# Kernel tuning notes

Hardware: AMD Instinct MI355X
Metric: run time of the kernel (lower is better)

Reference implementation:

```python
import jax, jax.numpy as jnp
import numpy as np

B, S, D, H = 2, 2048, 1024, 16
HD = D // H  # head_dim = 64


def setup_inputs() -> dict:
    key = jax.random.key(0)
    ks = jax.random.split(key, 9)
    scale = 0.02
    x = jax.random.normal(ks[0], (B, S, D), dtype=jnp.float32)
    wq = jax.random.normal(ks[1], (D, D), dtype=jnp.float32) * scale
    bq = jnp.zeros((D,), dtype=jnp.float32)
    wk = jax.random.normal(ks[2], (D, D), dtype=jnp.float32) * scale
    bk = jnp.zeros((D,), dtype=jnp.float32)
    wv = jax.random.normal(ks[3], (D, D), dtype=jnp.float32) * scale
    bv = jnp.zeros((D,), dtype=jnp.float32)
    wo = jax.random.normal(ks[4], (D, D), dtype=jnp.float32) * scale
    bo = jnp.zeros((D,), dtype=jnp.float32)
    # causal mask: 1.0 where key position is in the future of query position
    mask = jnp.triu(jnp.ones((S, S), dtype=jnp.float32), k=1)[None, None]  # [1,1,S,S]
    return {"x": x, "wq": wq, "bq": bq, "wk": wk, "bk": bk,
            "wv": wv, "bv": bv, "wo": wo, "bo": bo, "mask": mask}


def reference(x, wq, bq, wk, bk, wv, bv, wo, bo, mask):
    b, s, d = x.shape
    q = (x @ wq + bq).reshape(b, s, H, HD).transpose(0, 2, 1, 3)  # [b,h,s,hd]
    k = (x @ wk + bk).reshape(b, s, H, HD).transpose(0, 2, 1, 3)
    v = (x @ wv + bv).reshape(b, s, H, HD).transpose(0, 2, 1, 3)
    scores = jnp.einsum('bhqd,bhkd->bhqk', q, k) / jnp.sqrt(jnp.float32(HD))
    scores = scores + mask * (-1e9)
    probs = jax.nn.softmax(scores, axis=-1)
    out = jnp.einsum('bhqk,bhkd->bhqd', probs, v)
    out = out.transpose(0, 2, 1, 3).reshape(b, s, d)
    return out @ wo + bo
```

## Files before the change

### kernel.cpp

```cpp
#include <hip/hip_runtime.h>
#include <hip/hip_bf16.h>
#include <cstdint>

#define DEV static __device__ __forceinline__

typedef unsigned short u16t;
typedef __attribute__((ext_vector_type(4))) float f32x4;
typedef __attribute__((ext_vector_type(4))) unsigned short u16x4;
typedef __attribute__((ext_vector_type(8))) unsigned short u16x8;
typedef __attribute__((ext_vector_type(8))) __bf16 bf16x8;

DEV u16t f2bf(float f) {
  unsigned u = __builtin_bit_cast(unsigned, f);
  u += 0x7fffu + ((u >> 16) & 1u);
  return (u16t)(u >> 16);
}
DEV float bf2f(u16t h) {
  unsigned u = ((unsigned)h) << 16;
  return __builtin_bit_cast(float, u);
}

DEV void gload_lds16(const void* g, void* l) {
  __builtin_amdgcn_global_load_lds(
      (const __attribute__((address_space(1))) void*)g,
      (__attribute__((address_space(3))) void*)l, 16, 0, 0);
}

DEV bf16x8 ldsfrag(const u16t* p) {
  return __builtin_bit_cast(bf16x8, *(const u16x8*)p);
}

DEV void bsync() {
  asm volatile("" ::: "memory");
  __builtin_amdgcn_s_barrier();
  asm volatile("" ::: "memory");
}

__global__ __launch_bounds__(256) void k_convert_x(const float* __restrict__ x,
                                                   u16t* __restrict__ xb) {
  int i = (blockIdx.x * 256 + threadIdx.x) * 4;
  f32x4 v = *(const f32x4*)&x[i];
  u16x4 o;
#pragma unroll
  for (int j = 0; j < 4; ++j) o[j] = f2bf(v[j]);
  *(u16x4*)&xb[i] = o;
}

__global__ __launch_bounds__(256) void k_transw(const float* __restrict__ w0,
                                                const float* __restrict__ w1,
                                                const float* __restrict__ w2,
                                                const float* __restrict__ w3,
                                                u16t* __restrict__ qkvT,
                                                u16t* __restrict__ oT) {
  __shared__ float lds[64][68];
  int z = blockIdx.z;
  const float* W = (z == 0) ? w0 : (z == 1) ? w1 : (z == 2) ? w2 : w3;
  u16t* OUT = (z < 3) ? (qkvT + (size_t)z * 1024 * 1024) : oT;
  int k0 = blockIdx.x * 64, n0 = blockIdx.y * 64;
  int t = threadIdx.x;
  int kl = t >> 4, n4 = (t & 15) << 2;
#pragma unroll
  for (int p = 0; p < 4; ++p) {
    f32x4 v = *(const f32x4*)&W[(size_t)(k0 + kl + p * 16) * 1024 + n0 + n4];
    *(f32x4*)&lds[kl + p * 16][n4] = v;
  }
  __syncthreads();
  int nl = t >> 4, k4 = (t & 15) << 2;
#pragma unroll
  for (int p = 0; p < 4; ++p) {
    int n = nl + p * 16;
    u16x4 o;
#pragma unroll
    for (int i = 0; i < 4; ++i) o[i] = f2bf(lds[k4 + i][n]);
    *(u16x4*)&OUT[(size_t)(n0 + n) * 1024 + k0 + k4] = o;
  }
}

template <int MI, bool BF16_OUT, bool VSPLIT>
__global__ __launch_bounds__(256) void k_gemm_bt(const u16t* __restrict__ A,
                                                 const u16t* __restrict__ BT,
                                                 void* __restrict__ Cout,
                                                 const float* __restrict__ b0,
                                                 const float* __restrict__ b1,
                                                 const float* __restrict__ b2,
                                                 u16t* __restrict__ vt,
                                                 int M, int N, int K) {
  __shared__ u16t Al[2][MI * 32 * 64];
  __shared__ u16t Bl[2][128 * 64];
  const int tid = threadIdx.x;
  const int l = tid & 63;
  const int w = tid >> 6;
  const int m0 = blockIdx.x * (MI * 32), n0 = blockIdx.y * 128;
  const int wm = (w >> 1) * (MI * 16), wn = (w & 1) * 64;
  const int lm = l & 15, lh = l >> 4;
  f32x4 acc[MI][4] = {};

  auto stage = [&](int bb, int t) {
    const int k0 = t << 6;
#pragma unroll
    for (int s = 0; s < MI; ++s) {
      int c = s * 256 + tid;
      int row = c >> 3, slot = c & 7;
      int ks = k0 + (((slot ^ (row & 7)) & 7) << 3);
      gload_lds16(A + (size_t)(m0 + row) * K + ks, &Al[bb][c * 8]);
    }
#pragma unroll
    for (int s = 0; s < 4; ++s) {
      int c = s * 256 + tid;
      int row = c >> 3, slot = c & 7;
      int ks = k0 + (((slot ^ (row & 7)) & 7) << 3);
      gload_lds16(BT + (size_t)(n0 + row) * K + ks, &Bl[bb][c * 8]);
    }
  };

  const int nt = K >> 6;
  stage(0, 0);
  for (int t = 0; t < nt; ++t) {
    if (t + 1 < nt) {
      stage((t + 1) & 1, t + 1);
      if (MI == 2)
        asm volatile("s_waitcnt vmcnt(6)" ::: "memory");
      else
        asm volatile("s_waitcnt vmcnt(8)" ::: "memory");
    } else {
      asm volatile("s_waitcnt vmcnt(0)" ::: "memory");
    }
    bsync();
    const int buf = t & 1;

#pragma unroll
    for (int kk = 0; kk < 2; ++kk) {
      bf16x8 af[MI], bfr[4];
#pragma unroll
      for (int i = 0; i < MI; ++i) {
        int ra = wm + i * 16 + lm;
        int sa = (kk * 4 + lh) ^ (ra & 7);
        af[i] = ldsfrag(&Al[buf][ra * 64 + sa * 8]);
      }
#pragma unroll
      for (int i = 0; i < 4; ++i) {
        int rb = wn + i * 16 + lm;
        int sb = (kk * 4 + lh) ^ (rb & 7);
        bfr[i] = ldsfrag(&Bl[buf][rb * 64 + sb * 8]);
      }
#pragma unroll
      for (int i = 0; i < MI; ++i)
#pragma unroll
        for (int j = 0; j < 4; ++j)
          acc[i][j] = __builtin_amdgcn_mfma_f32_16x16x32_bf16(af[i], bfr[j],
                                                              acc[i][j], 0, 0, 0);
    }
    bsync();
  }

  if (!VSPLIT || (n0 + wn) < 2048) {
#pragma unroll
    for (int i = 0; i < MI; ++i) {
      int row = m0 + wm + i * 16 + (lh << 2);
#pragma unroll
      for (int j = 0; j < 4; ++j) {
        int col = n0 + wn + j * 16 + lm;
        const float* bp = (col < 1024) ? b0 : ((col < 2048) ? b1 : b2);
        float bias = bp[col & 1023];
#pragma unroll
        for (int r = 0; r < 4; ++r) {
          float v = acc[i][j][r] + bias;
          if (BF16_OUT)
            ((u16t*)Cout)[(size_t)(row + r) * N + col] = f2bf(v);
          else
            ((float*)Cout)[(size_t)(row + r) * N + col] = v;
        }
      }
    }
  } else {
#pragma unroll
    for (int i = 0; i < MI; ++i) {
      int row = m0 + wm + i * 16 + (lh << 2);
      int bidx = row >> 11, s0 = row & 2047;
#pragma unroll
      for (int j = 0; j < 4; ++j) {
        int col = n0 + wn + j * 16 + lm;
        int d = col - 2048;
        int hh = d >> 6, dd = d & 63;
        float bias = b2[d];
        u16x4 o;
#pragma unroll
        for (int r = 0; r < 4; ++r) o[r] = f2bf(acc[i][j][r] + bias);
        *(u16x4*)&vt[((size_t)((bidx * 16 + hh) * 64 + dd)) * 2048 + s0] = o;
      }
    }
  }
}

__global__ __launch_bounds__(256, 4) void k_attn(const u16t* qkv,
                                                 const u16t* __restrict__ vt,
                                                 u16t* __restrict__ outp,
                                                 u16t* scratch) {
  __shared__ u16t Kl[4096];
  __shared__ u16t Vl[4096];
  __shared__ u16t Pl[4][1024];
  const int tid = threadIdx.x, l = tid & 63, w = tid >> 6;
  const int lm = l & 15, lh = l >> 4;
  const int bh = blockIdx.x, b = bh >> 4, h = bh & 15;
  const int y = blockIdx.y;
  const int zone = y >> 4, j = y & 15;
  const int qt = (zone == 0) ? ((j < 8) ? j : 23 - j) : ((j < 8) ? 16 + j : 39 - j);
  const int half = (qt >> 1) + 1;
  const int t0 = (zone == 2) ? half : 0;
  const int t1 = (zone == 1) ? half : qt + 1;
  const int q0 = qt * 64;
  const int qrow = q0 + w * 16 + lm;

  bf16x8 aq[2];
#pragma unroll
  for (int kk = 0; kk < 2; ++kk) {
    const u16t* src = qkv + (size_t)(b * 2048 + qrow) * 3072 + h * 64 + kk * 32 + lh * 8;
    u16x8 v = *(const u16x8*)src;
    u16x8 o;
#pragma unroll
    for (int e = 0; e < 8; ++e) o[e] = f2bf(bf2f(v[e]) * 0.1803368801f);
    aq[kk] = __builtin_bit_cast(bf16x8, o);
  }

  float lsum = 0.f;
  f32x4 aco[4] = {};

  const u16t* Kg = qkv + (size_t)b * 2048 * 3072 + 1024 + h * 64;
  const u16t* Vg = vt + (size_t)bh * 64 * 2048;
  u16t* Pw = &Pl[w][0];

  auto stage = [&](int t) {
#pragma unroll
    for (int s = 0; s < 2; ++s) {
      int c = s * 256 + tid;
      int row = c >> 3, col = ((c & 7) ^ (row & 7)) << 3;
      gload_lds16(Kg + (size_t)(t * 64 + row) * 3072 + col, &Kl[c * 8]);
    }
#pragma unroll
    for (int s = 0; s < 2; ++s) {
      int c = s * 256 + tid;
      int row = c >> 3, col = ((c & 7) ^ (row & 7)) << 3;
      gload_lds16(Vg + (size_t)row * 2048 + t * 64 + col, &Vl[c * 8]);
    }
  };

  for (int t = t0; t < t1; ++t) {
    stage(t);
    asm volatile("s_waitcnt vmcnt(0)" ::: "memory");
    bsync();

    f32x4 accs[4] = {};
#pragma unroll
    for (int kk = 0; kk < 2; ++kk) {
      bf16x8 ak[4];
#pragma unroll
      for (int nk = 0; nk < 4; ++nk) {
        int rk = nk * 16 + lm;
        int s16 = (kk * 4 + lh) ^ (rk & 7);
        ak[nk] = ldsfrag(&Kl[rk * 64 + s16 * 8]);
      }
      __builtin_amdgcn_s_setprio(1);
#pragma unroll
      for (int nk = 0; nk < 4; ++nk)
        accs[nk] = __builtin_amdgcn_mfma_f32_16x16x32_bf16(ak[nk], aq[kk],
                                                           accs[nk], 0, 0, 0);
      __builtin_amdgcn_s_setprio(0);
    }

    if (t == qt) {
#pragma unroll
      for (int nk = 0; nk < 4; ++nk)
#pragma unroll
        for (int r = 0; r < 4; ++r) {
          int kvpos = t * 64 + nk * 16 + lh * 4 + r;
          if (kvpos > qrow) accs[nk][r] = -1e30f;
        }
    }

#pragma unroll
    for (int nk = 0; nk < 4; ++nk) {
      float p0 = exp2f(accs[nk][0]);
      float p1 = exp2f(accs[nk][1]);
      float p2 = exp2f(accs[nk][2]);
      float p3 = exp2f(accs[nk][3]);
      lsum += (p0 + p1) + (p2 + p3);
      unsigned wlo, whi;
      asm("v_cvt_pk_bf16_f32 %0, %1, %2" : "=v"(wlo) : "v"(p0), "v"(p1));
      asm("v_cvt_pk_bf16_f32 %0, %1, %2" : "=v"(whi) : "v"(p2), "v"(p3));
      int off = lm * 64 + ((((2 * nk + (lh >> 1)) ^ (lm & 7)) & 7) << 3) +
                ((lh & 1) << 2);
      *(uint2*)&Pw[off] = make_uint2(wlo, whi);
    }

#pragma unroll
    for (int kk = 0; kk < 2; ++kk) {
      int s16p = (kk * 4 + lh) ^ (lm & 7);
      bf16x8 ap = ldsfrag(&Pw[lm * 64 + s16p * 8]);
      __builtin_amdgcn_s_setprio(1);
#pragma unroll
      for (int nd = 0; nd < 4; ++nd) {
        int rv = nd * 16 + lm;
        int s16v = (kk * 4 + lh) ^ (rv & 7);
        bf16x8 bv = ldsfrag(&Vl[rv * 64 + s16v * 8]);
        aco[nd] = __builtin_amdgcn_mfma_f32_16x16x32_bf16(ap, bv, aco[nd], 0, 0, 0);
      }
      __builtin_amdgcn_s_setprio(0);
    }

    bsync();
  }

  lsum += __shfl_xor(lsum, 16);
  lsum += __shfl_xor(lsum, 32);

  if (zone == 0) {
    float inv = 1.0f / lsum;
#pragma unroll
    for (int r = 0; r < 4; ++r) {
      float ir = __shfl(inv, lh * 4 + r);
      int row = q0 + w * 16 + lh * 4 + r;
#pragma unroll
      for (int nd = 0; nd < 4; ++nd) {
        int col = h * 64 + nd * 16 + lm;
        outp[(size_t)(b * 2048 + row) * 1024 + col] = f2bf(aco[nd][r] * ir);
      }
    }
  } else {
#pragma unroll
    for (int r = 0; r < 4; ++r) {
      int row = q0 + w * 16 + lh * 4 + r;
#pragma unroll
      for (int nd = 0; nd < 4; ++nd) {
        int col = nd * 16 + lm;
        u16t v = f2bf(aco[nd][r]);
        if (zone == 1)
          outp[(size_t)(b * 2048 + row) * 1024 + h * 64 + col] = v;
        else
          scratch[(size_t)(b * 2048 + row - 1024) * 3072 + 2048 + h * 64 + col] = v;
      }
    }
    if (l < 16) {
      int row = q0 + w * 16 + l;
      float* ml = (float*)&scratch[(size_t)(b * 2048 + row) * 3072 + 2048];
      ml[h * 2 + (zone - 1)] = lsum;
    }
  }
}

__global__ __launch_bounds__(256) void k_merge(const u16t* __restrict__ scratch,
                                               u16t* __restrict__ outp) {
  int x = blockIdx.x;
  int b = x >> 10, rr = x & 1023, row = 1024 + rr;
  int c4 = threadIdx.x * 4;
  int h = c4 >> 6;
  const float* ml = (const float*)&scratch[(size_t)(b * 2048 + row) * 3072 + 2048];
  float inv = 1.0f / (ml[h * 2] + ml[h * 2 + 1]);
  u16t* op = &outp[(size_t)(b * 2048 + row) * 1024 + c4];
  const u16t* o1 = &scratch[(size_t)(b * 2048 + rr) * 3072 + 2048 + c4];
  u16x4 a = *(const u16x4*)op;
  u16x4 bb = *(const u16x4*)o1;
  u16x4 o;
#pragma unroll
  for (int i = 0; i < 4; ++i) o[i] = f2bf((bf2f(a[i]) + bf2f(bb[i])) * inv);
  *(u16x4*)op = o;
}

extern "C" void kernel_launch(void* const* d_in, const int* in_sizes, int n_in,
                              void* d_out, int out_size, void* d_ws, size_t ws_size,
                              hipStream_t stream) {
  const float* x = (const float*)d_in[0];
  const float* wq = (const float*)d_in[1];
  const float* bq = (const float*)d_in[2];
  const float* wk = (const float*)d_in[3];
  const float* bk = (const float*)d_in[4];
  const float* wv = (const float*)d_in[5];
  const float* bv = (const float*)d_in[6];
  const float* wo = (const float*)d_in[7];
  const float* bo = (const float*)d_in[8];

  char* ws = (char*)d_ws;
  u16t* xb = (u16t*)ws;
  u16t* wqkvT = (u16t*)(ws + (8u << 20));
  u16t* woT = (u16t*)(ws + (14u << 20));
  u16t* qkv = (u16t*)(ws + (16u << 20));
  u16t* vt = (u16t*)(ws + (40u << 20));
  u16t* attn_out = xb;

  k_convert_x<<<4096, 256, 0, stream>>>(x, xb);
  k_transw<<<dim3(16, 16, 4), 256, 0, stream>>>(wq, wk, wv, wo, wqkvT, woT);
  k_gemm_bt<2, true, true><<<dim3(64, 24), 256, 0, stream>>>(
      xb, wqkvT, qkv, bq, bk, bv, vt, 4096, 3072, 1024);
  k_attn<<<dim3(32, 48), 256, 0, stream>>>(qkv, vt, attn_out, qkv);
  k_merge<<<2048, 256, 0, stream>>>(qkv, attn_out);
  k_gemm_bt<2, false, false><<<dim3(64, 8), 256, 0, stream>>>(
      attn_out, woT, d_out, bo, bo, bo, nullptr, 4096, 1024, 1024);
}
```

Baseline: 107.8 us.

## Double attention query tile to 128 rows per block, two 16-row subtiles per wave

The attention kernel now handles 128 query rows per block, so each wave processes two 16-row query subtiles that share every K/V tile staged in LDS and every K/V fragment read. This halves the number of K/V global loads and LDS fragment reads per query row and halves the grid. Waves skip KV tiles lying entirely above their causal diagonal. In exchange, register use per thread roughly doubles (occupancy hint lowered to 2 blocks per SM) and fewer blocks are available for load balancing.

New measurement: 107.7 us. No clear change (-0.1%).

```diff
diff --git a/kernel.cpp b/kernel.cpp
--- a/kernel.cpp
+++ b/kernel.cpp
@@ -192,42 +192,45 @@
   }
 }
 
-__global__ __launch_bounds__(256, 4) void k_attn(const u16t* qkv,
+__global__ __launch_bounds__(256, 2) void k_attn(const u16t* qkv,
                                                  const u16t* __restrict__ vt,
                                                  u16t* __restrict__ outp,
                                                  u16t* scratch) {
   __shared__ u16t Kl[4096];
   __shared__ u16t Vl[4096];
-  __shared__ u16t Pl[4][1024];
+  __shared__ u16t Pl[4][2][1024];
   const int tid = threadIdx.x, l = tid & 63, w = tid >> 6;
   const int lm = l & 15, lh = l >> 4;
   const int bh = blockIdx.x, b = bh >> 4, h = bh & 15;
   const int y = blockIdx.y;
-  const int zone = y >> 4, j = y & 15;
-  const int qt = (zone == 0) ? ((j < 8) ? j : 23 - j) : ((j < 8) ? 16 + j : 39 - j);
-  const int half = (qt >> 1) + 1;
-  const int t0 = (zone == 2) ? half : 0;
-  const int t1 = (zone == 1) ? half : qt + 1;
-  const int q0 = qt * 64;
-  const int qrow = q0 + w * 16 + lm;
-
-  bf16x8 aq[2];
-#pragma unroll
-  for (int kk = 0; kk < 2; ++kk) {
-    const u16t* src = qkv + (size_t)(b * 2048 + qrow) * 3072 + h * 64 + kk * 32 + lh * 8;
-    u16x8 v = *(const u16x8*)src;
-    u16x8 o;
-#pragma unroll
-    for (int e = 0; e < 8; ++e) o[e] = f2bf(bf2f(v[e]) * 0.1803368801f);
-    aq[kk] = __builtin_bit_cast(bf16x8, o);
-  }
-
-  float lsum = 0.f;
-  f32x4 aco[4] = {};
+  const int zone = y >> 3, j = y & 7;
+  const int qt = (zone == 0) ? j : (15 - j);
+  const int q0 = qt * 128;
+  const int halfn = qt + 1;
+  const int t0 = (zone == 2) ? halfn : 0;
+  const int t1 = (zone == 1) ? halfn : (2 * qt + 2);
+  const int qbase = q0 + w * 32;
+
+  bf16x8 aq[2][2];
+#pragma unroll
+  for (int qm = 0; qm < 2; ++qm)
+#pragma unroll
+    for (int kk = 0; kk < 2; ++kk) {
+      const u16t* src = qkv + (size_t)(b * 2048 + qbase + qm * 16 + lm) * 3072 +
+                        h * 64 + kk * 32 + lh * 8;
+      u16x8 v = *(const u16x8*)src;
+      u16x8 o;
+#pragma unroll
+      for (int e = 0; e < 8; ++e) o[e] = f2bf(bf2f(v[e]) * 0.1803368801f);
+      aq[qm][kk] = __builtin_bit_cast(bf16x8, o);
+    }
+
+  float lsum[2] = {0.f, 0.f};
+  f32x4 aco[2][4] = {};
+  const int qr0 = qbase + lm, qr1 = qbase + 16 + lm;
 
   const u16t* Kg = qkv + (size_t)b * 2048 * 3072 + 1024 + h * 64;
   const u16t* Vg = vt + (size_t)bh * 64 * 2048;
-  u16t* Pw = &Pl[w][0];
 
   auto stage = [&](int t) {
 #pragma unroll
@@ -249,100 +252,124 @@
     asm volatile("s_waitcnt vmcnt(0)" ::: "memory");
     bsync();
 
-    f32x4 accs[4] = {};
-#pragma unroll
-    for (int kk = 0; kk < 2; ++kk) {
-      bf16x8 ak[4];
-#pragma unroll
-      for (int nk = 0; nk < 4; ++nk) {
-        int rk = nk * 16 + lm;
-        int s16 = (kk * 4 + lh) ^ (rk & 7);
-        ak[nk] = ldsfrag(&Kl[rk * 64 + s16 * 8]);
-      }
-      __builtin_amdgcn_s_setprio(1);
-#pragma unroll
-      for (int nk = 0; nk < 4; ++nk)
-        accs[nk] = __builtin_amdgcn_mfma_f32_16x16x32_bf16(ak[nk], aq[kk],
-                                                           accs[nk], 0, 0, 0);
-      __builtin_amdgcn_s_setprio(0);
-    }
-
-    if (t == qt) {
-#pragma unroll
-      for (int nk = 0; nk < 4; ++nk)
-#pragma unroll
-        for (int r = 0; r < 4; ++r) {
-          int kvpos = t * 64 + nk * 16 + lh * 4 + r;
-          if (kvpos > qrow) accs[nk][r] = -1e30f;
-        }
-    }
-
-#pragma unroll
-    for (int nk = 0; nk < 4; ++nk) {
-      float p0 = exp2f(accs[nk][0]);
-      float p1 = exp2f(accs[nk][1]);
-      float p2 = exp2f(accs[nk][2]);
-      float p3 = exp2f(accs[nk][3]);
-      lsum += (p0 + p1) + (p2 + p3);
-      unsigned wlo, whi;
-      asm("v_cvt_pk_bf16_f32 %0, %1, %2" : "=v"(wlo) : "v"(p0), "v"(p1));
-      asm("v_cvt_pk_bf16_f32 %0, %1, %2" : "=v"(whi) : "v"(p2), "v"(p3));
-      int off = lm * 64 + ((((2 * nk + (lh >> 1)) ^ (lm & 7)) & 7) << 3) +
-                ((lh & 1) << 2);
-      *(uint2*)&Pw[off] = make_uint2(wlo, whi);
-    }
-
-#pragma unroll
-    for (int kk = 0; kk < 2; ++kk) {
-      int s16p = (kk * 4 + lh) ^ (lm & 7);
-      bf16x8 ap = ldsfrag(&Pw[lm * 64 + s16p * 8]);
-      __builtin_amdgcn_s_setprio(1);
-#pragma unroll
-      for (int nd = 0; nd < 4; ++nd) {
-        int rv = nd * 16 + lm;
-        int s16v = (kk * 4 + lh) ^ (rv & 7);
-        bf16x8 bv = ldsfrag(&Vl[rv * 64 + s16v * 8]);
-        aco[nd] = __builtin_amdgcn_mfma_f32_16x16x32_bf16(ap, bv, aco[nd], 0, 0, 0);
-      }
-      __builtin_amdgcn_s_setprio(0);
+    if (t * 64 <= qbase + 31) {
+      f32x4 accs[2][4] = {};
+#pragma unroll
+      for (int kk = 0; kk < 2; ++kk) {
+        bf16x8 ak[4];
+#pragma unroll
+        for (int nk = 0; nk < 4; ++nk) {
+          int rk = nk * 16 + lm;
+          int s16 = (kk * 4 + lh) ^ (rk & 7);
+          ak[nk] = ldsfrag(&Kl[rk * 64 + s16 * 8]);
+        }
+        __builtin_amdgcn_s_setprio(1);
+#pragma unroll
+        for (int nk = 0; nk < 4; ++nk) {
+          accs[0][nk] = __builtin_amdgcn_mfma_f32_16x16x32_bf16(
+              ak[nk], aq[0][kk], accs[0][nk], 0, 0, 0);
+          accs[1][nk] = __builtin_amdgcn_mfma_f32_16x16x32_bf16(
+              ak[nk], aq[1][kk], accs[1][nk], 0, 0, 0);
+        }
+        __builtin_amdgcn_s_setprio(0);
+      }
+
+      if (t * 64 + 63 > qbase) {
+#pragma unroll
+        for (int nk = 0; nk < 4; ++nk)
+#pragma unroll
+          for (int r = 0; r < 4; ++r) {
+            int kvpos = t * 64 + nk * 16 + lh * 4 + r;
+            if (kvpos > qr0) accs[0][nk][r] = -1e30f;
+            if (kvpos > qr1) accs[1][nk][r] = -1e30f;
+          }
+      }
+
+#pragma unroll
+      for (int qm = 0; qm < 2; ++qm) {
+        u16t* Pw = &Pl[w][qm][0];
+#pragma unroll
+        for (int nk = 0; nk < 4; ++nk) {
+          float p0 = exp2f(accs[qm][nk][0]);
+          float p1 = exp2f(accs[qm][nk][1]);
+          float p2 = exp2f(accs[qm][nk][2]);
+          float p3 = exp2f(accs[qm][nk][3]);
+          lsum[qm] += (p0 + p1) + (p2 + p3);
+          unsigned wlo, whi;
+          asm("v_cvt_pk_bf16_f32 %0, %1, %2" : "=v"(wlo) : "v"(p0), "v"(p1));
+          asm("v_cvt_pk_bf16_f32 %0, %1, %2" : "=v"(whi) : "v"(p2), "v"(p3));
+          int off = lm * 64 + ((((2 * nk + (lh >> 1)) ^ (lm & 7)) & 7) << 3) +
+                    ((lh & 1) << 2);
+          *(uint2*)&Pw[off] = make_uint2(wlo, whi);
+        }
+      }
+
+#pragma unroll
+      for (int kk = 0; kk < 2; ++kk) {
+        int sp = (kk * 4 + lh) ^ (lm & 7);
+        bf16x8 ap0 = ldsfrag(&Pl[w][0][lm * 64 + sp * 8]);
+        bf16x8 ap1 = ldsfrag(&Pl[w][1][lm * 64 + sp * 8]);
+        __builtin_amdgcn_s_setprio(1);
+#pragma unroll
+        for (int nd = 0; nd < 4; ++nd) {
+          int rv = nd * 16 + lm;
+          int sv = (kk * 4 + lh) ^ (rv & 7);
+          bf16x8 bv = ldsfrag(&Vl[rv * 64 + sv * 8]);
+          aco[0][nd] =
+              __builtin_amdgcn_mfma_f32_16x16x32_bf16(ap0, bv, aco[0][nd], 0, 0, 0);
+          aco[1][nd] =
+              __builtin_amdgcn_mfma_f32_16x16x32_bf16(ap1, bv, aco[1][nd], 0, 0, 0);
+        }
+        __builtin_amdgcn_s_setprio(0);
+      }
     }
 
     bsync();
   }
 
-  lsum += __shfl_xor(lsum, 16);
-  lsum += __shfl_xor(lsum, 32);
+#pragma unroll
+  for (int qm = 0; qm < 2; ++qm) {
+    lsum[qm] += __shfl_xor(lsum[qm], 16);
+    lsum[qm] += __shfl_xor(lsum[qm], 32);
+  }
 
   if (zone == 0) {
-    float inv = 1.0f / lsum;
-#pragma unroll
-    for (int r = 0; r < 4; ++r) {
-      float ir = __shfl(inv, lh * 4 + r);
-      int row = q0 + w * 16 + lh * 4 + r;
-#pragma unroll
-      for (int nd = 0; nd < 4; ++nd) {
-        int col = h * 64 + nd * 16 + lm;
-        outp[(size_t)(b * 2048 + row) * 1024 + col] = f2bf(aco[nd][r] * ir);
+#pragma unroll
+    for (int qm = 0; qm < 2; ++qm) {
+      float inv = 1.0f / lsum[qm];
+#pragma unroll
+      for (int r = 0; r < 4; ++r) {
+        float ir = __shfl(inv, lh * 4 + r);
+        int row = qbase + qm * 16 + lh * 4 + r;
+#pragma unroll
+        for (int nd = 0; nd < 4; ++nd) {
+          int col = h * 64 + nd * 16 + lm;
+          outp[(size_t)(b * 2048 + row) * 1024 + col] = f2bf(aco[qm][nd][r] * ir);
+        }
       }
     }
   } else {
 #pragma unroll
-    for (int r = 0; r < 4; ++r) {
-      int row = q0 + w * 16 + lh * 4 + r;
-#pragma unroll
-      for (int nd = 0; nd < 4; ++nd) {
-        int col = nd * 16 + lm;
-        u16t v = f2bf(aco[nd][r]);
-        if (zone == 1)
-          outp[(size_t)(b * 2048 + row) * 1024 + h * 64 + col] = v;
-        else
-          scratch[(size_t)(b * 2048 + row - 1024) * 3072 + 2048 + h * 64 + col] = v;
-      }
-    }
+    for (int qm = 0; qm < 2; ++qm)
+#pragma unroll
+      for (int r = 0; r < 4; ++r) {
+        int row = qbase + qm * 16 + lh * 4 + r;
+#pragma unroll
+        for (int nd = 0; nd < 4; ++nd) {
+          int col = nd * 16 + lm;
+          u16t v = f2bf(aco[qm][nd][r]);
+          if (zone == 1)
+            outp[(size_t)(b * 2048 + row) * 1024 + h * 64 + col] = v;
+          else
+            scratch[(size_t)(b * 2048 + row - 1024) * 3072 + 2048 + h * 64 + col] = v;
+        }
+      }
     if (l < 16) {
-      int row = q0 + w * 16 + l;
-      float* ml = (float*)&scratch[(size_t)(b * 2048 + row) * 3072 + 2048];
-      ml[h * 2 + (zone - 1)] = lsum;
+      float* ml0 = (float*)&scratch[(size_t)(b * 2048 + qbase + l) * 3072 + 2048];
+      ml0[h * 2 + (zone - 1)] = lsum[0];
+      float* ml1 =
+          (float*)&scratch[(size_t)(b * 2048 + qbase + 16 + l) * 3072 + 2048];
+      ml1[h * 2 + (zone - 1)] = lsum[1];
     }
   }
 }
@@ -390,7 +417,7 @@
   k_transw<<<dim3(16, 16, 4), 256, 0, stream>>>(wq, wk, wv, wo, wqkvT, woT);
   k_gemm_bt<2, true, true><<<dim3(64, 24), 256, 0, stream>>>(
       xb, wqkvT, qkv, bq, bk, bv, vt, 4096, 3072, 1024);
-  k_attn<<<dim3(32, 48), 256, 0, stream>>>(qkv, vt, attn_out, qkv);
+  k_attn<<<dim3(32, 24), 256, 0, stream>>>(qkv, vt, attn_out, qkv);
   k_merge<<<2048, 256, 0, stream>>>(qkv, attn_out);
   k_gemm_bt<2, false, false><<<dim3(64, 8), 256, 0, stream>>>(
       attn_out, woT, d_out, bo, bo, bo, nullptr, 4096, 1024, 1024);
```
